# Performance work log

Measured on AMD Instinct MI355X. Metric: run time of the kernel, lower is better.

## Reference

```python
import jax, jax.numpy as jnp
import numpy as np

IGNORE_INDEX = -100
B, S, D, V = 2, 1024, 1024, 128000


def setup_inputs() -> dict:
    key = jax.random.key(0)
    k1, k2, k3 = jax.random.split(key, 3)
    hidden = jax.random.normal(k1, (B, S, D), dtype=jnp.float32)
    # output projection weight (torchtune model.output: Linear(D, V, bias=False))
    weight = jax.random.normal(k2, (V, D), dtype=jnp.float32) * (D ** -0.5)
    targets = jax.random.randint(k3, (B, S), 0, V, dtype=jnp.int32)
    return {"hidden": hidden, "weight": weight, "targets": targets}


def reference(hidden, weight, targets):
    # mask ignored tokens (original masks before projection; same math)
    mask = targets != IGNORE_INDEX                                  # [B,S]
    safe_t = jnp.where(mask, targets, 0)                            # in-range gather indices
    logits = jnp.einsum('bsd,vd->bsv', hidden, weight)              # [B,S,V]
    logits = logits.astype(jnp.float32)                             # matches logits.float()
    logZ = jax.nn.logsumexp(logits, axis=-1)                        # [B,S]
    tgt_logit = jnp.take_along_axis(logits, safe_t[..., None], axis=-1)[..., 0]
    nll = logZ - tgt_logit                                          # per-token CE
    total_loss = jnp.sum(jnp.where(mask, nll, 0.0))                 # reduction='sum' over non-ignored
    n = jnp.sum(mask).astype(jnp.float32)
    return jnp.where(n == 0, total_loss, total_loss / jnp.maximum(n, 1.0))
```

## Files before the change

kernel.cpp:

```cpp
#include <hip/hip_runtime.h>
#include <hip/hip_bf16.h>
#include <hip/hip_fp8.h>
#include <math.h>

#define IGNORE_INDEX (-100)

static constexpr int Dc = 1024, Vc = 128000;
static constexpr int Mrows = 2048;
static constexpr int Kdim = 1024;
static constexpr int NKT = Kdim / 32;
static constexpr int NCHUNK = Vc / 64;

typedef float f32x4_t __attribute__((ext_vector_type(4)));

__global__ void cast_f32_fp8_pack(const float* __restrict__ in, uchar* __restrict__ out,
                                  size_t n8) {
  size_t i = (size_t)blockIdx.x * blockDim.x + threadIdx.x;
  size_t stride = (size_t)gridDim.x * blockDim.x;
  for (; i < n8; i += stride) {
    int lane = (int)(i & 63);
    size_t ftile = i >> 6;
    size_t rt = ftile >> 5;
    int kt = (int)(ftile & 31);
    size_t row = rt * 16 + (lane & 15);
    int k = kt * 32 + (lane >> 4) * 8;
    const float* p = in + row * Kdim + k;
    float4 v0 = *reinterpret_cast<const float4*>(p);
    float4 v1 = *reinterpret_cast<const float4*>(p + 4);
    union { uchar b[8]; unsigned long long u; } o;
    o.b[0] = __hip_fp8_e4m3(v0.x).__x; o.b[1] = __hip_fp8_e4m3(v0.y).__x;
    o.b[2] = __hip_fp8_e4m3(v0.z).__x; o.b[3] = __hip_fp8_e4m3(v0.w).__x;
    o.b[4] = __hip_fp8_e4m3(v1.x).__x; o.b[5] = __hip_fp8_e4m3(v1.y).__x;
    o.b[6] = __hip_fp8_e4m3(v1.z).__x; o.b[7] = __hip_fp8_e4m3(v1.w).__x;
    reinterpret_cast<unsigned long long*>(out)[i] = o.u;
  }
}

__global__ void tgt_kernel(const float* __restrict__ hidden, const float* __restrict__ weight,
                           const int* __restrict__ targets, float* __restrict__ tgt) {
  int row = blockIdx.x * 4 + (threadIdx.x >> 6);
  int lane = threadIdx.x & 63;
  if (row >= Mrows) return;
  int t = targets[row];
  float sum = 0.f;
  if (t != IGNORE_INDEX) {
    const float* h = hidden + (size_t)row * Kdim;
    const float* wv = weight + (size_t)t * Kdim;
    for (int k = lane * 4; k < Kdim; k += 64 * 4) {
      float4 a = *reinterpret_cast<const float4*>(h + k);
      float4 b = *reinterpret_cast<const float4*>(wv + k);
      sum += a.x * b.x + a.y * b.y + a.z * b.z + a.w * b.w;
    }
  }
  #pragma unroll
  for (int d = 1; d < 64; d <<= 1) sum += __shfl_xor(sum, d);
  if (lane == 0) tgt[row] = sum;
}

#define MFMA_FP8(A, B, C) __builtin_amdgcn_mfma_f32_16x16x32_fp8_fp8((A), (B), (C), 0, 0, 0)

__global__ __launch_bounds__(512, 4) void gemm_lse_fp8(const uchar* __restrict__ Apk,
                                                       const uchar* __restrict__ Bpk,
                                                       float2* __restrict__ part) {
  const int tid = threadIdx.x;
  const int wid = tid >> 6, lane = tid & 63;
  const int wr = wid >> 2, wc = wid & 3;
  const int l15 = lane & 15, l16 = lane >> 4;
  const int bid = blockIdx.x;
  const int mb = bid & 15;
  const int nb = bid >> 4;

  const uchar* aF[4]; const uchar* bF[4];
  #pragma unroll
  for (int mi = 0; mi < 4; ++mi)
    aF[mi] = Apk + ((size_t)(mb * 8 + wr * 4 + mi) * NKT) * 512 + lane * 8;
  #pragma unroll
  for (int ni = 0; ni < 4; ++ni)
    bF[ni] = Bpk + ((size_t)(nb * 16 + wc * 4 + ni) * NKT) * 512 + lane * 8;

  f32x4_t acc[4][4];
  #pragma unroll
  for (int i = 0; i < 4; ++i)
    #pragma unroll
    for (int j = 0; j < 4; ++j)
      acc[i][j] = (f32x4_t){0.f, 0.f, 0.f, 0.f};

  long aA[4], bA[4], aB[4], bB[4];
  #pragma unroll
  for (int mi = 0; mi < 4; ++mi) aA[mi] = *reinterpret_cast<const long*>(aF[mi]);
  #pragma unroll
  for (int ni = 0; ni < 4; ++ni) bA[ni] = *reinterpret_cast<const long*>(bF[ni]);

  #pragma unroll 1
  for (int t = 0; t < NKT; t += 2) {
    if (t + 1 < NKT) {
      #pragma unroll
      for (int mi = 0; mi < 4; ++mi)
        aB[mi] = *reinterpret_cast<const long*>(aF[mi] + (t + 1) * 512);
      #pragma unroll
      for (int ni = 0; ni < 4; ++ni)
        bB[ni] = *reinterpret_cast<const long*>(bF[ni] + (t + 1) * 512);
    }
    __builtin_amdgcn_s_setprio(1);
    #pragma unroll
    for (int mi = 0; mi < 4; ++mi)
      #pragma unroll
      for (int ni = 0; ni < 4; ++ni)
        acc[mi][ni] = MFMA_FP8(aA[mi], bA[ni], acc[mi][ni]);
    __builtin_amdgcn_s_setprio(0);
    if (t + 2 < NKT) {
      #pragma unroll
      for (int mi = 0; mi < 4; ++mi)
        aA[mi] = *reinterpret_cast<const long*>(aF[mi] + (t + 2) * 512);
      #pragma unroll
      for (int ni = 0; ni < 4; ++ni)
        bA[ni] = *reinterpret_cast<const long*>(bF[ni] + (t + 2) * 512);
    }
    __builtin_amdgcn_s_setprio(1);
    #pragma unroll
    for (int mi = 0; mi < 4; ++mi)
      #pragma unroll
      for (int ni = 0; ni < 4; ++ni)
        acc[mi][ni] = MFMA_FP8(aB[mi], bB[ni], acc[mi][ni]);
    __builtin_amdgcn_s_setprio(0);
  }

  const int chunk = nb * 4 + wc;
  #pragma unroll
  for (int mi = 0; mi < 4; ++mi) {
    #pragma unroll
    for (int j = 0; j < 4; ++j) {
      float v0 = acc[mi][0][j], v1 = acc[mi][1][j], v2 = acc[mi][2][j], v3 = acc[mi][3][j];
      float mloc = fmaxf(fmaxf(v0, v1), fmaxf(v2, v3));
      #pragma unroll
      for (int d = 1; d < 16; d <<= 1) mloc = fmaxf(mloc, __shfl_xor(mloc, d));
      float sloc = __expf(v0 - mloc) + __expf(v1 - mloc) +
                   __expf(v2 - mloc) + __expf(v3 - mloc);
      #pragma unroll
      for (int d = 1; d < 16; d <<= 1) sloc += __shfl_xor(sloc, d);
      if (l15 == 0) {
        int grow = mb * 128 + wr * 64 + mi * 16 + l16 * 4 + j;
        part[(size_t)grow * NCHUNK + chunk] = make_float2(mloc, sloc);
      }
    }
  }
}

__device__ __forceinline__ void merge_ms(float& m, float& s, float m2, float s2) {
  if (m2 > m) { s = s * __expf(m - m2) + s2; m = m2; }
  else        { s += s2 * __expf(m2 - m); }
}

__global__ void lse_reduce(const float2* __restrict__ part, const float* __restrict__ tgt,
                           const int* __restrict__ targets, float* __restrict__ nll) {
  int row = blockIdx.x;
  const float2* p = part + (size_t)row * NCHUNK;
  float m = -INFINITY, s = 0.f;
  for (int c = threadIdx.x; c < NCHUNK; c += blockDim.x) {
    float2 v = p[c];
    merge_ms(m, s, v.x, v.y);
  }
  #pragma unroll
  for (int d = 1; d < 64; d <<= 1) {
    float m2 = __shfl_xor(m, d), s2 = __shfl_xor(s, d);
    merge_ms(m, s, m2, s2);
  }
  __shared__ float sm[4], ss[4];
  int wid = threadIdx.x >> 6, lane = threadIdx.x & 63;
  if (lane == 0) { sm[wid] = m; ss[wid] = s; }
  __syncthreads();
  if (threadIdx.x == 0) {
    #pragma unroll
    for (int w2 = 1; w2 < 4; ++w2) merge_ms(m, s, sm[w2], ss[w2]);
    int t = targets[row];
    float out = 0.f;
    if (t != IGNORE_INDEX) out = m + logf(s) - tgt[row];
    nll[row] = out;
  }
}

__global__ void final_kernel(const float* __restrict__ nll, const int* __restrict__ targets,
                             float* __restrict__ out) {
  float sum = 0.f, cnt = 0.f;
  for (int i = threadIdx.x; i < Mrows; i += 64) {
    sum += nll[i];
    cnt += (targets[i] != IGNORE_INDEX) ? 1.f : 0.f;
  }
  #pragma unroll
  for (int d = 1; d < 64; d <<= 1) {
    sum += __shfl_xor(sum, d);
    cnt += __shfl_xor(cnt, d);
  }
  if (threadIdx.x == 0)
    out[0] = (cnt == 0.f) ? sum : sum / fmaxf(cnt, 1.f);
}

extern "C" void kernel_launch(void* const* d_in, const int* in_sizes, int n_in,
                              void* d_out, int out_size, void* d_ws, size_t ws_size,
                              hipStream_t stream) {
  const float* hidden = (const float*)d_in[0];
  const float* weight = (const float*)d_in[1];
  const int* targets  = (const int*)d_in[2];
  float* out = (float*)d_out;

  char* ws = (char*)d_ws;
  size_t off = 0;
  uchar* w8 = (uchar*)(ws + off); off += (size_t)Vc * Dc;
  uchar* h8 = (uchar*)(ws + off); off += (size_t)Mrows * Dc;
  float2* part = (float2*)(ws + off); off += (size_t)Mrows * NCHUNK * sizeof(float2);
  float* tgt = (float*)(ws + off); off += Mrows * sizeof(float);
  float* nll = (float*)(ws + off); off += Mrows * sizeof(float);
  (void)ws_size; (void)in_sizes; (void)n_in; (void)out_size;

  cast_f32_fp8_pack<<<2048, 256, 0, stream>>>(weight, w8, (size_t)Vc * Dc / 8);
  cast_f32_fp8_pack<<<256, 256, 0, stream>>>(hidden, h8, (size_t)Mrows * Dc / 8);
  tgt_kernel<<<Mrows / 4, 256, 0, stream>>>(hidden, weight, targets, tgt);

  gemm_lse_fp8<<<8000, 512, 0, stream>>>(h8, w8, part);

  lse_reduce<<<Mrows, 256, 0, stream>>>(part, tgt, targets, nll);
  final_kernel<<<1, 64, 0, stream>>>(nll, targets, out);
}
```

Baseline: 650.1 us.

## Switch GEMM to 16x16x128 scaled MFMA with LDS double-buffered direct loads

Replaces the 16x16x32 fp8 MFMA loop, which loaded operands straight from global memory into registers, with the MI355X scaled 16x16x128 f8f6f4 MFMA using unit scales. Operand tiles are staged into a double-buffered LDS area through global_load_lds, and the fp8 packing layout is changed to match the new 128-wide K fragments. Blocks shrink to 256 threads covering 128x128 tiles, so twice as many blocks are launched. This cuts the number of MFMA instructions and gives coalesced 16-byte loads, at the cost of a barrier per K step and 64KB of LDS per block.

New measurement: 1.958 ms. 201% more time.

```diff
diff --git a/kernel.cpp b/kernel.cpp
--- a/kernel.cpp
+++ b/kernel.cpp
@@ -8,9 +8,11 @@
 static constexpr int Dc = 1024, Vc = 128000;
 static constexpr int Mrows = 2048;
 static constexpr int Kdim = 1024;
-static constexpr int NKT = Kdim / 32;
+static constexpr int NT128 = Kdim / 128;
 static constexpr int NCHUNK = Vc / 64;
 
+typedef int i32x4 __attribute__((ext_vector_type(4)));
+typedef int i32x8 __attribute__((ext_vector_type(8)));
 typedef float f32x4_t __attribute__((ext_vector_type(4)));
 
 __global__ void cast_f32_fp8_pack(const float* __restrict__ in, uchar* __restrict__ out,
@@ -18,12 +20,16 @@
   size_t i = (size_t)blockIdx.x * blockDim.x + threadIdx.x;
   size_t stride = (size_t)gridDim.x * blockDim.x;
   for (; i < n8; i += stride) {
-    int lane = (int)(i & 63);
-    size_t ftile = i >> 6;
-    size_t rt = ftile >> 5;
-    int kt = (int)(ftile & 31);
+    size_t q = i * 8;
+    size_t ftile = q >> 11;
+    int rem = (int)(q & 2047);
+    int chunk = rem >> 10;
+    int lane = (rem >> 4) & 63;
+    int sub0 = rem & 15;
+    size_t rt = ftile >> 3;
+    int kt = (int)(ftile & 7);
     size_t row = rt * 16 + (lane & 15);
-    int k = kt * 32 + (lane >> 4) * 8;
+    int k = kt * 128 + (lane >> 4) * 32 + chunk * 16 + sub0;
     const float* p = in + row * Kdim + k;
     float4 v0 = *reinterpret_cast<const float4*>(p);
     float4 v1 = *reinterpret_cast<const float4*>(p + 4);
@@ -57,26 +63,32 @@
   if (lane == 0) tgt[row] = sum;
 }
 
-#define MFMA_FP8(A, B, C) __builtin_amdgcn_mfma_f32_16x16x32_fp8_fp8((A), (B), (C), 0, 0, 0)
-
-__global__ __launch_bounds__(512, 4) void gemm_lse_fp8(const uchar* __restrict__ Apk,
-                                                       const uchar* __restrict__ Bpk,
-                                                       float2* __restrict__ part) {
+#define MXFMA(A, B, C) __builtin_amdgcn_mfma_scale_f32_16x16x128_f8f6f4( \
+    (A), (B), (C), 0, 0, 0, 0x7F7F7F7F, 0, 0x7F7F7F7F)
+#define GLDS(g, l) __builtin_amdgcn_global_load_lds( \
+    (const __attribute__((address_space(1))) void*)(g), \
+    (__attribute__((address_space(3))) void*)(l), 16, 0, 0)
+
+__global__ __launch_bounds__(256, 2) void gemm_lse_mx(const uchar* __restrict__ Apk,
+                                                      const uchar* __restrict__ Bpk,
+                                                      float2* __restrict__ part) {
+  __shared__ uchar lds[2][32768];
   const int tid = threadIdx.x;
   const int wid = tid >> 6, lane = tid & 63;
-  const int wr = wid >> 2, wc = wid & 3;
+  const int wr = wid >> 1, wc = wid & 1;
   const int l15 = lane & 15, l16 = lane >> 4;
   const int bid = blockIdx.x;
   const int mb = bid & 15;
   const int nb = bid >> 4;
 
-  const uchar* aF[4]; const uchar* bF[4];
-  #pragma unroll
-  for (int mi = 0; mi < 4; ++mi)
-    aF[mi] = Apk + ((size_t)(mb * 8 + wr * 4 + mi) * NKT) * 512 + lane * 8;
-  #pragma unroll
-  for (int ni = 0; ni < 4; ++ni)
-    bF[ni] = Bpk + ((size_t)(nb * 16 + wc * 4 + ni) * NKT) * 512 + lane * 8;
+  const uchar* sgA[4]; const uchar* sgB[4];
+  #pragma unroll
+  for (int j = 0; j < 4; ++j) {
+    int c = j * 256 + tid;
+    int f = c >> 7, idx = c & 127;
+    sgA[j] = Apk + ((size_t)(mb * 8 + f) * NT128) * 2048 + idx * 16;
+    sgB[j] = Bpk + ((size_t)(nb * 8 + f) * NT128) * 2048 + idx * 16;
+  }
 
   f32x4_t acc[4][4];
   #pragma unroll
@@ -85,47 +97,54 @@
     for (int j = 0; j < 4; ++j)
       acc[i][j] = (f32x4_t){0.f, 0.f, 0.f, 0.f};
 
-  long aA[4], bA[4], aB[4], bB[4];
-  #pragma unroll
-  for (int mi = 0; mi < 4; ++mi) aA[mi] = *reinterpret_cast<const long*>(aF[mi]);
-  #pragma unroll
-  for (int ni = 0; ni < 4; ++ni) bA[ni] = *reinterpret_cast<const long*>(bF[ni]);
-
-  #pragma unroll 1
-  for (int t = 0; t < NKT; t += 2) {
-    if (t + 1 < NKT) {
-      #pragma unroll
-      for (int mi = 0; mi < 4; ++mi)
-        aB[mi] = *reinterpret_cast<const long*>(aF[mi] + (t + 1) * 512);
-      #pragma unroll
-      for (int ni = 0; ni < 4; ++ni)
-        bB[ni] = *reinterpret_cast<const long*>(bF[ni] + (t + 1) * 512);
+  #define STAGE(bufp, kt) do { \
+    _Pragma("unroll") \
+    for (int j = 0; j < 4; ++j) { \
+      int c = j * 256 + tid; \
+      GLDS(sgA[j] + (size_t)(kt) * 2048, (bufp) + c * 16); \
+      GLDS(sgB[j] + (size_t)(kt) * 2048, (bufp) + 16384 + c * 16); \
+    } \
+  } while (0)
+
+  STAGE(lds[0], 0);
+  asm volatile("s_waitcnt vmcnt(0)" ::: "memory");
+  __builtin_amdgcn_s_barrier();
+
+  for (int t = 0; t < NT128; ++t) {
+    const int buf = t & 1;
+    if (t + 1 < NT128) STAGE(lds[buf ^ 1], t + 1);
+    const uchar* Ar = lds[buf];
+    const uchar* Br = lds[buf] + 16384;
+    i32x8 a8[4], b8[4];
+    #pragma unroll
+    for (int mi = 0; mi < 4; ++mi) {
+      const uchar* base = Ar + (wr * 4 + mi) * 2048 + lane * 16;
+      i32x4 lo = *reinterpret_cast<const i32x4*>(base);
+      i32x4 hi = *reinterpret_cast<const i32x4*>(base + 1024);
+      a8[mi] = __builtin_shufflevector(lo, hi, 0, 1, 2, 3, 4, 5, 6, 7);
+    }
+    #pragma unroll
+    for (int ni = 0; ni < 4; ++ni) {
+      const uchar* base = Br + (wc * 4 + ni) * 2048 + lane * 16;
+      i32x4 lo = *reinterpret_cast<const i32x4*>(base);
+      i32x4 hi = *reinterpret_cast<const i32x4*>(base + 1024);
+      b8[ni] = __builtin_shufflevector(lo, hi, 0, 1, 2, 3, 4, 5, 6, 7);
     }
     __builtin_amdgcn_s_setprio(1);
     #pragma unroll
     for (int mi = 0; mi < 4; ++mi)
       #pragma unroll
       for (int ni = 0; ni < 4; ++ni)
-        acc[mi][ni] = MFMA_FP8(aA[mi], bA[ni], acc[mi][ni]);
+        acc[mi][ni] = MXFMA(a8[mi], b8[ni], acc[mi][ni]);
     __builtin_amdgcn_s_setprio(0);
-    if (t + 2 < NKT) {
-      #pragma unroll
-      for (int mi = 0; mi < 4; ++mi)
-        aA[mi] = *reinterpret_cast<const long*>(aF[mi] + (t + 2) * 512);
-      #pragma unroll
-      for (int ni = 0; ni < 4; ++ni)
-        bA[ni] = *reinterpret_cast<const long*>(bF[ni] + (t + 2) * 512);
-    }
-    __builtin_amdgcn_s_setprio(1);
-    #pragma unroll
-    for (int mi = 0; mi < 4; ++mi)
-      #pragma unroll
-      for (int ni = 0; ni < 4; ++ni)
-        acc[mi][ni] = MFMA_FP8(aB[mi], bB[ni], acc[mi][ni]);
-    __builtin_amdgcn_s_setprio(0);
-  }
-
-  const int chunk = nb * 4 + wc;
+    if (t + 1 < NT128) {
+      asm volatile("s_waitcnt vmcnt(0)" ::: "memory");
+      __builtin_amdgcn_s_barrier();
+    }
+  }
+  #undef STAGE
+
+  const int chunk = nb * 2 + wc;
   #pragma unroll
   for (int mi = 0; mi < 4; ++mi) {
     #pragma unroll
@@ -216,7 +235,7 @@
   cast_f32_fp8_pack<<<256, 256, 0, stream>>>(hidden, h8, (size_t)Mrows * Dc / 8);
   tgt_kernel<<<Mrows / 4, 256, 0, stream>>>(hidden, weight, targets, tgt);
 
-  gemm_lse_fp8<<<8000, 512, 0, stream>>>(h8, w8, part);
+  gemm_lse_mx<<<16000, 256, 0, stream>>>(h8, w8, part);
 
   lse_reduce<<<Mrows, 256, 0, stream>>>(part, tgt, targets, nll);
   final_kernel<<<1, 64, 0, stream>>>(nll, targets, out);
```
